# Kernel optimization log

Measured on AMD Instinct MI355X. Metric: run time of the kernel, lower is better.

## Reference

```python
import jax, jax.numpy as jnp
import numpy as np

B = 2
C = 256
NA = 3  # aspect ratios per location
IMG_H, IMG_W = 800, 1216
FEAT_SHAPES = [(200, 304), (100, 152), (50, 76), (25, 38), (13, 19)]
STRIDES = [4, 8, 16, 32, 64]
SIZES = [32, 64, 128, 256, 512]
RATIOS = np.array([0.5, 1.0, 2.0])
PRE_NMS = 1000
POST_NMS = 1000
NMS_TH = 0.7
MIN_SIZE = 1e-3
BBOX_CLIP = float(np.log(1000.0 / 16.0))
NUM_PER_LEVEL = [h * w * NA for h, w in FEAT_SHAPES]


def _make_anchors():
    out = []
    for (h, w), stride, size in zip(FEAT_SHAPES, STRIDES, SIZES):
        hr = np.sqrt(RATIOS)
        wr = 1.0 / hr
        ws, hs = wr * size, hr * size
        base = np.stack([-ws / 2, -hs / 2, ws / 2, hs / 2], 1)  # [NA,4]
        yy, xx = np.meshgrid(np.arange(h) * stride, np.arange(w) * stride, indexing='ij')
        shifts = np.stack([xx.ravel(), yy.ravel(), xx.ravel(), yy.ravel()], 1)  # [h*w,4]
        out.append((shifts[:, None, :] + base[None, :, :]).reshape(-1, 4))
    return jnp.asarray(np.concatenate(out, 0), jnp.float32)  # [A,4]

ANCHORS = _make_anchors()
# level id of each selected (per-level top-k) anchor is static
LEVELS_SEL = jnp.asarray(
    np.concatenate([np.full(min(PRE_NMS, a), i) for i, a in enumerate(NUM_PER_LEVEL)]),
    jnp.float32)


def conv2d(x, w, b, pad):
    y = jax.lax.conv_general_dilated(x, w, (1, 1), [(pad, pad), (pad, pad)],
                                     dimension_numbers=('NCHW', 'OIHW', 'NCHW'))
    return y + b[None, :, None, None]


def decode(reg, anc):
    # BoxCoder.decode with weights (1,1,1,1)
    wa = anc[..., 2] - anc[..., 0]
    ha = anc[..., 3] - anc[..., 1]
    cxa = anc[..., 0] + 0.5 * wa
    cya = anc[..., 1] + 0.5 * ha
    dx, dy = reg[..., 0], reg[..., 1]
    dw = jnp.minimum(reg[..., 2], BBOX_CLIP)
    dh = jnp.minimum(reg[..., 3], BBOX_CLIP)
    cx = dx * wa + cxa
    cy = dy * ha + cya
    w = jnp.exp(dw) * wa
    h = jnp.exp(dh) * ha
    return jnp.stack([cx - 0.5 * w, cy - 0.5 * h, cx + 0.5 * w, cy + 0.5 * h], -1)


def _nms_select(boxes, scores, valid, lvl_offsets):
    # batched_nms via per-level coordinate offset trick; greedy NMS over IoU matrix
    b = boxes + lvl_offsets[:, None]
    s = jnp.where(valid, scores, -jnp.inf)
    order = jnp.argsort(-s)
    bs = b[order]
    keep = valid[order]
    area = (bs[:, 2] - bs[:, 0]) * (bs[:, 3] - bs[:, 1])
    lt = jnp.maximum(bs[:, None, :2], bs[None, :, :2])
    rb = jnp.minimum(bs[:, None, 2:], bs[None, :, 2:])
    wh = jnp.clip(rb - lt, 0.0)
    inter = wh[..., 0] * wh[..., 1]
    iou = inter / (area[:, None] + area[None, :] - inter + 1e-9)
    K = boxes.shape[0]
    ar = jnp.arange(K)

    def body(i, keep):
        sup = keep[i] & (iou[i] > NMS_TH) & (ar > i)
        return keep & ~sup

    keep = jax.lax.fori_loop(0, K, body, keep)
    keep_orig = jnp.zeros(K, bool).at[order].set(keep)
    ms = jnp.where(keep_orig, scores, -jnp.inf)
    top_s, idx = jax.lax.top_k(ms, POST_NMS)
    return idx, jnp.isfinite(top_s)


def reference(feat0, feat1, feat2, feat3, feat4, conv_w, conv_b, cls_w, cls_b, box_w, box_b):
    logit_l, reg_l = [], []
    for f in (feat0, feat1, feat2, feat3, feat4):
        t = jax.nn.relu(conv2d(f, conv_w, conv_b, 1))
        l = conv2d(t, cls_w, cls_b, 0)   # [B,NA,H,W]
        r = conv2d(t, box_w, box_b, 0)   # [B,NA*4,H,W]
        _, _, H, W = l.shape
        logit_l.append(l.transpose(0, 2, 3, 1).reshape(B, -1))                        # HWC order
        reg_l.append(r.reshape(B, NA, 4, H, W).transpose(0, 3, 4, 1, 2).reshape(B, -1, 4))
    logits = jnp.concatenate(logit_l, 1)   # [B,A]
    regs = jnp.concatenate(reg_l, 1)       # [B,A,4]
    proposals = decode(regs, ANCHORS[None])  # [B,A,4]

    # per-level top-k (pre-NMS)
    sel, off = [], 0
    for a in NUM_PER_LEVEL:
        k = min(PRE_NMS, a)
        _, idx = jax.lax.top_k(logits[:, off:off + a], k)
        sel.append(idx + off)
        off += a
    sel = jnp.concatenate(sel, 1)          # [B,Ksel]
    bi = jnp.arange(B)[:, None]
    sc = logits[bi, sel]
    bx = proposals[bi, sel]

    # clip to image, remove small boxes (mask)
    x0 = jnp.clip(bx[..., 0], 0.0, float(IMG_W))
    y0 = jnp.clip(bx[..., 1], 0.0, float(IMG_H))
    x1 = jnp.clip(bx[..., 2], 0.0, float(IMG_W))
    y1 = jnp.clip(bx[..., 3], 0.0, float(IMG_H))
    bx = jnp.stack([x0, y0, x1, y1], -1)
    valid = ((x1 - x0) >= MIN_SIZE) & ((y1 - y0) >= MIN_SIZE)
    offs = LEVELS_SEL * (float(max(IMG_W, IMG_H)) + 1.0)

    idx2, vout = jax.vmap(lambda b_, s_, v_: _nms_select(b_, s_, v_, offs))(
        jax.lax.stop_gradient(bx), jax.lax.stop_gradient(sc), valid)

    boxes_out = jnp.take_along_axis(bx, idx2[..., None], 1)   # [B,POST_NMS,4]
    scores_out = jnp.take_along_axis(sc, idx2, 1)             # [B,POST_NMS]
    boxes_out = jnp.where(vout[..., None], boxes_out, 0.0)
    scores_out = jnp.where(vout, scores_out, -1e9)
    return boxes_out, scores_out


def setup_inputs() -> dict:
    key = jax.random.key(0)
    ks = jax.random.split(key, 9)
    inp = {}
    for i, (h, w) in enumerate(FEAT_SHAPES):
        inp[f'feat{i}'] = jax.random.normal(ks[i], (B, C, h, w), jnp.float32)
    inp['conv_w'] = jax.random.normal(ks[5], (C, C, 3, 3), jnp.float32) * 0.01
    inp['conv_b'] = jnp.zeros((C,), jnp.float32)
    inp['cls_w'] = jax.random.normal(ks[6], (NA, C, 1, 1), jnp.float32) * 0.01
    inp['cls_b'] = jnp.zeros((NA,), jnp.float32)
    inp['box_w'] = jax.random.normal(ks[7], (NA * 4, C, 1, 1), jnp.float32) * 0.01
    inp['box_b'] = jnp.zeros((NA * 4,), jnp.float32)
    return inp
```

## Files before the change

kernel.cpp:

```cpp
#include <hip/hip_runtime.h>
#include <hip/hip_fp16.h>
#include <stdint.h>
#include <math.h>

typedef unsigned int uint;
typedef unsigned short ushort;
typedef unsigned long long ull;
typedef __attribute__((ext_vector_type(8))) _Float16 f16x8;
typedef __attribute__((ext_vector_type(4))) float f32x4;

#define BATCH 2
#define ATOTAL 242991
#define KSEL 4741
#define NW 75
#define POST_NMS 1000
#define WB_ELEMS (2*8*3*3*2*8*64*8)
#define NPAIRS 2850

__device__ __constant__ int dLoff[5]  = {0,182400,228000,239400,242250};
__device__ __constant__ int dCount[5] = {182400,45600,11400,2850,741};
__device__ __constant__ int dSeg[5]   = {0,1000,2000,3000,4000};
__device__ __constant__ int dSegK[5]  = {1000,1000,1000,1000,741};
__device__ __constant__ int dHc[5]     = {200,100,50,25,13};
__device__ __constant__ int dWc[5]     = {304,152,76,38,19};
__device__ __constant__ int dTilesX[5] = {19,10,5,3,2};
__device__ __constant__ int dCumT[6]   = {0,475,605,640,652,656};
__device__ __constant__ int dStrideC[5]= {4,8,16,32,64};
__device__ __constant__ int dSizeC[5]  = {32,64,128,256,512};

__device__ __forceinline__ uint fkey(float f) {
    uint u = __float_as_uint(f);
    return (u & 0x80000000u) ? ~u : (u | 0x80000000u);
}
__device__ __forceinline__ ushort h2u(__half h) {
    union { __half h; ushort u; } x; x.h = h; return x.u;
}

__global__ __launch_bounds__(256) void wt_kernel(const float* __restrict__ conv_w,
                                                 ushort* __restrict__ wB) {
    int t = blockIdx.x * 256 + threadIdx.x;
    if (t >= WB_ELEMS) return;
    int e    = t & 7;
    int lane = (t >> 3) & 63;
    int nt   = (t >> 9) & 7;
    int pl   = (t >> 12) & 1;
    int r    = t >> 13;
    int dx = r % 3; r /= 3;
    int dy = r % 3; r /= 3;
    int icblk = r & 7;
    int ocg = r >> 3;
    int oc = ocg * 128 + nt * 16 + (lane & 15);
    int ic = icblk * 32 + ((lane >> 4) << 3) + e;
    float v = conv_w[(size_t)oc * 2304 + ic * 9 + dy * 3 + dx];
    __half h = __float2half(v);
    float rr = (v - __half2float(h)) * 1024.0f;
    __half m = __float2half(rr);
    wB[t] = (pl == 0) ? h2u(h) : h2u(m);
}

__global__ __launch_bounds__(512) void conv_mfma_all(
    const float* __restrict__ f0, const float* __restrict__ f1,
    const float* __restrict__ f2, const float* __restrict__ f3,
    const float* __restrict__ f4, const ushort* __restrict__ wB,
    const float* __restrict__ conv_b,
    const float* __restrict__ cls_w, const float* __restrict__ cls_b,
    const float* __restrict__ box_w, const float* __restrict__ box_b,
    float* __restrict__ scoresA, float* __restrict__ boxesA)
{
    const int bidx = blockIdx.x;
    const int b    = blockIdx.y;
    const int tid  = threadIdx.x;

    int lvl = 0;
#pragma unroll
    for (int l = 1; l < 5; ++l) if (bidx >= dCumT[l]) lvl = l;
    const int tile   = bidx - dCumT[lvl];
    const int H      = dHc[lvl], W = dWc[lvl];
    const int TILESX = dTilesX[lvl];
    const int ty0    = (tile / TILESX) * 8;
    const int tx0    = (tile % TILESX) * 16;
    const int HW     = H * W;
    const float* feat = (lvl == 0) ? f0 : (lvl == 1) ? f1 : (lvl == 2) ? f2 : (lvl == 3) ? f3 : f4;
    const float* fb = feat + (size_t)b * 256 * HW;

    __shared__ __align__(16) char uni[72192];
    ushort* halo = (ushort*)uni;
    ushort* ldsB = (ushort*)(uni + 23040);
    float*  tS   = (float*)uni;
    float*  hw2  = (float*)(uni + 32768);
    double* houtD= (double*)uni;

    const int lane = tid & 63, wave = tid >> 6;
    const int wm = wave >> 1, wn = wave & 1;
    const int g = lane >> 4, col = lane & 15;
    const int laneA = g * 1440 + col * 8;

    int  hdst[12]; int hoff[12]; bool hval[12];
#pragma unroll
    for (int j = 0; j < 12; ++j) {
        int e = tid + j * 512;
        hdst[j] = -1; hoff[j] = 0; hval[j] = false;
        if (e < 5760) {
            int ic = e / 180, rem = e - ic * 180;
            int hrow = rem / 18, hcol = rem - hrow * 18;
            int gy = ty0 + hrow - 1, gx = tx0 + hcol - 1;
            hdst[j] = (((ic >> 3) * 10 + hrow) * 18 + hcol) * 8 + (ic & 7);
            if (gy >= 0 && gy < H && gx >= 0 && gx < W) {
                hval[j] = true; hoff[j] = ic * HW + gy * W + gx;
            }
        }
    }

    double hacc[4] = {0,0,0,0};

    uint4 Br0, Br1, Br2, Br3, Br4, Br5;
    {
        const uint4* gq = (const uint4*)wB;
        Br0 = gq[tid];        Br1 = gq[tid + 512];
        Br2 = gq[tid + 1024]; Br3 = gq[tid + 1536];
        Br4 = gq[tid + 2048]; Br5 = gq[tid + 2560];
    }

#pragma unroll 1
    for (int ocg = 0; ocg < 2; ++ocg) {
        f32x4 accH[2][4], accM[2][4];
#pragma unroll
        for (int mi = 0; mi < 2; ++mi)
#pragma unroll
            for (int ni = 0; ni < 4; ++ni) {
                accH[mi][ni] = (f32x4){0.f, 0.f, 0.f, 0.f};
                accM[mi][ni] = (f32x4){0.f, 0.f, 0.f, 0.f};
            }

#pragma unroll 1
        for (int s = 0; s < 24; ++s) {
            const int icblk = s / 3;
            const int dy    = s - icblk * 3;

            __syncthreads();
            if (dy == 0) {
                float hv[12];
                const float* fcb = fb + (size_t)icblk * 32 * HW;
#pragma unroll
                for (int j = 0; j < 12; ++j)
                    hv[j] = hval[j] ? fcb[hoff[j]] : 0.f;
#pragma unroll
                for (int j = 0; j < 12; ++j) {
                    if (hdst[j] >= 0) {
                        float v = hv[j];
                        __half h = __float2half(v);
                        float rr = (v - __half2float(h)) * 1024.0f;
                        __half m = __float2half(rr);
                        int li = hdst[j];
                        halo[li] = h2u(h); halo[5760 + li] = h2u(m);
                    }
                }
            }
            {
                uint4* lq = (uint4*)ldsB;
                lq[tid] = Br0;         lq[tid + 512]  = Br1;
                lq[tid + 1024] = Br2;  lq[tid + 1536] = Br3;
                lq[tid + 2048] = Br4;  lq[tid + 2560] = Br5;
            }
            __syncthreads();
            {
                int gstep = ocg * 24 + s + 1;
                if (gstep < 48) {
                    const uint4* gq = (const uint4*)(wB + (size_t)gstep * 24576);
                    Br0 = gq[tid];        Br1 = gq[tid + 512];
                    Br2 = gq[tid + 1024]; Br3 = gq[tid + 1536];
                    Br4 = gq[tid + 2048]; Br5 = gq[tid + 2560];
                }
            }
#pragma unroll 1
            for (int dx = 0; dx < 3; ++dx) {
                f16x8 Ah[2], Am[2];
                const int abase = laneA + dx * 8 + (2 * wm + dy) * 144;
#pragma unroll
                for (int mi = 0; mi < 2; ++mi) {
                    Ah[mi] = *(const f16x8*)(halo + abase + mi * 144);
                    Am[mi] = *(const f16x8*)(halo + 5760 + abase + mi * 144);
                }
#pragma unroll
                for (int ni = 0; ni < 4; ++ni) {
                    const int nt = 4 * wn + ni;
                    f16x8 Bh = *(const f16x8*)(ldsB + (size_t)(dx * 16 + nt) * 512 + lane * 8);
                    f16x8 Bm = *(const f16x8*)(ldsB + (size_t)(dx * 16 + 8 + nt) * 512 + lane * 8);
                    __builtin_amdgcn_s_setprio(1);
#pragma unroll
                    for (int mi = 0; mi < 2; ++mi) {
                        f32x4 cH = accH[mi][ni];
                        f32x4 cM = accM[mi][ni];
                        cH = __builtin_amdgcn_mfma_f32_16x16x32_f16(Ah[mi], Bh, cH, 0, 0, 0);
                        cM = __builtin_amdgcn_mfma_f32_16x16x32_f16(Ah[mi], Bm, cM, 0, 0, 0);
                        cM = __builtin_amdgcn_mfma_f32_16x16x32_f16(Am[mi], Bh, cM, 0, 0, 0);
                        accH[mi][ni] = cH;
                        accM[mi][ni] = cM;
                    }
                    __builtin_amdgcn_s_setprio(0);
                }
            }
        }
        __syncthreads();
        float cb[4];
#pragma unroll
        for (int ni = 0; ni < 4; ++ni)
            cb[ni] = conv_b[ocg * 128 + (4 * wn + ni) * 16 + col];

#pragma unroll 1
        for (int s2 = 0; s2 < 2; ++s2) {
            if (wn == s2) {
#pragma unroll
                for (int mi = 0; mi < 2; ++mi) {
#pragma unroll
                    for (int r = 0; r < 4; ++r) {
                        int px = (2 * wm + mi) * 16 + 4 * g + r;
                        int sw = px & 15;
#pragma unroll
                        for (int ni = 0; ni < 4; ++ni) {
                            int slot = (ni * 4 + (col >> 2)) ^ sw;
                            float val = accH[mi][ni][r] + accM[mi][ni][r] * 0.0009765625f;
                            tS[px * 64 + slot * 4 + (col & 3)] =
                                fmaxf(val + cb[ni], 0.f);
                        }
                    }
                }
            }
            if (tid < 256) {
                const int oc2 = tid >> 2;
                const int h0  = (tid & 3) * 4;
                const int oc  = ocg * 128 + s2 * 64 + oc2;
                float vv[4];
#pragma unroll
                for (int q = 0; q < 4; ++q) {
                    int h = h0 + q;
                    vv[q] = (h < 3) ? cls_w[h * 256 + oc]
                          : (h < 15) ? box_w[(h - 3) * 256 + oc] : 0.f;
                }
                *(float4*)&hw2[oc2 * 16 + h0] = make_float4(vv[0], vv[1], vv[2], vv[3]);
            }
            __syncthreads();
            {
                const int px = tid & 127;
                const int hh = tid >> 7;
                const int sw = px & 15;
#pragma unroll 1
                for (int j4 = 0; j4 < 16; ++j4) {
                    float4 t4 = *(const float4*)&tS[px * 64 + (j4 ^ sw) * 4];
                    float tv[4] = {t4.x, t4.y, t4.z, t4.w};
#pragma unroll
                    for (int jj = 0; jj < 4; ++jj) {
                        const float* hb = &hw2[(j4 * 4 + jj) * 16 + hh * 4];
                        float4 h0 = *(const float4*)hb;
                        double tv_d = (double)tv[jj];
                        hacc[0] += tv_d * (double)h0.x;
                        hacc[1] += tv_d * (double)h0.y;
                        hacc[2] += tv_d * (double)h0.z;
                        hacc[3] += tv_d * (double)h0.w;
                    }
                }
            }
            __syncthreads();
        }
    }

    {
        const int px = tid & 127;
        const int hh = tid >> 7;
#pragma unroll
        for (int j = 0; j < 4; ++j) houtD[px * 16 + hh * 4 + j] = hacc[j];
    }
    __syncthreads();

    if (tid < 128) {
        const int px = tid;
        const int gy = ty0 + (px >> 4);
        const int gx = tx0 + (px & 15);
        if (gy < H && gx < W) {
            const int STRIDE = dStrideC[lvl];
            const int SZ     = dSizeC[lvl];
            const int LOFF   = dLoff[lvl];
#pragma unroll 1
            for (int a = 0; a < 3; ++a) {
                double score = houtD[px * 16 + a] + (double)cls_b[a];
                double rg0 = houtD[px * 16 + 3 + a * 4 + 0] + (double)box_b[a * 4 + 0];
                double rg1 = houtD[px * 16 + 3 + a * 4 + 1] + (double)box_b[a * 4 + 1];
                double rg2 = houtD[px * 16 + 3 + a * 4 + 2] + (double)box_b[a * 4 + 2];
                double rg3 = houtD[px * 16 + 3 + a * 4 + 3] + (double)box_b[a * 4 + 3];
                double ratio = (a == 0) ? 0.5 : ((a == 1) ? 1.0 : 2.0);
                double hr = sqrt(ratio), wr = 1.0 / hr;
                double wsd = wr * (double)SZ, hsd = hr * (double)SZ;
                double sx = (double)(gx * STRIDE), sy = (double)(gy * STRIDE);
                float ax0 = (float)(sx - 0.5 * wsd);
                float ay0 = (float)(sy - 0.5 * hsd);
                float ax1 = (float)(sx + 0.5 * wsd);
                float ay1 = (float)(sy + 0.5 * hsd);
                double wa = (double)ax1 - (double)ax0, ha = (double)ay1 - (double)ay0;
                double cxa = (double)ax0 + 0.5 * wa, cya = (double)ay0 + 0.5 * ha;
                double dwv = fmin(rg2, 4.135166556742356);
                double dhv = fmin(rg3, 4.135166556742356);
                double cx = rg0 * wa + cxa, cy = rg1 * ha + cya;
                double w = exp(dwv) * wa, h = exp(dhv) * ha;
                double x0 = cx - 0.5 * w, y0 = cy - 0.5 * h;
                double x1 = cx + 0.5 * w, y1 = cy + 0.5 * h;
                x0 = fmin(fmax(x0, 0.0), 1216.0);
                y0 = fmin(fmax(y0, 0.0), 800.0);
                x1 = fmin(fmax(x1, 0.0), 1216.0);
                y1 = fmin(fmax(y1, 0.0), 800.0);
                int gidx = LOFF + (gy * W + gx) * 3 + a;
                scoresA[(size_t)b * ATOTAL + gidx] = (float)score;
                float4 bx = make_float4((float)x0, (float)y0, (float)x1, (float)y1);
                *(float4*)&boxesA[((size_t)b * ATOTAL + gidx) * 4] = bx;
            }
        }
    }
}

__global__ __launch_bounds__(1024) void topk_kernel(
    const float* __restrict__ scoresA, const float* __restrict__ boxesA,
    float* __restrict__ selScore, float* __restrict__ selBox,
    int* __restrict__ selValid, int* __restrict__ selAnchor)
{
    const int lvl = blockIdx.x, b = blockIdx.y;
    const int n = dCount[lvl], loff = dLoff[lvl], seg = dSeg[lvl], k = dSegK[lvl];
    const float* sc = scoresA + (size_t)b * ATOTAL + loff;
    const int tid = threadIdx.x;

    float* oS = selScore + b * KSEL;
    float* oB = selBox + (size_t)b * KSEL * 4;
    int* oV = selValid + b * KSEL;
    int* oA = selAnchor + b * KSEL;

    auto emit = [&](int slot, int i) {
        int g = loff + i;
        float s = sc[i];
        float4 bx = *(const float4*)&boxesA[((size_t)b * ATOTAL + g) * 4];
        oS[seg + slot] = s;
        *(float4*)&oB[(size_t)(seg + slot) * 4] = bx;
        oV[seg + slot] = ((bx.z - bx.x) >= 1e-3f && (bx.w - bx.y) >= 1e-3f) ? 1 : 0;
        oA[seg + slot] = g;
    };

    if (n <= k) {
        for (int i = tid; i < n; i += 1024) emit(i, i);
        return;
    }

    __shared__ uint hist[2048];
    __shared__ uint suf[2][1024];
    __shared__ uint sh_bin, sh_krem;
    __shared__ uint cntG, cntE;
    __shared__ int stash[64];

    uint krem = (uint)k;
    uint prefix = 0;
    for (int pass = 0; pass < 3; ++pass) {
        for (int e = tid; e < 2048; e += 1024) hist[e] = 0;
        __syncthreads();
        for (int i = tid; i < n; i += 1024) {
            uint key = fkey(sc[i]);
            uint bin; bool sel;
            if (pass == 0)      { sel = true;                      bin = key >> 21; }
            else if (pass == 1) { sel = ((key >> 21) == prefix);   bin = (key >> 10) & 0x7FFu; }
            else                { sel = ((key >> 10) == prefix);   bin = key & 0x3FFu; }
            if (sel) atomicAdd(&hist[bin], 1u);
        }
        __syncthreads();
        {
            const int nb = (pass == 2) ? 1024 : 2048;
            uint pv = 0;
            if (2 * tid < nb)     pv += hist[2 * tid];
            if (2 * tid + 1 < nb) pv += hist[2 * tid + 1];
            suf[0][tid] = pv;
            __syncthreads();
            int src = 0;
#pragma unroll
            for (int off2 = 1; off2 < 1024; off2 <<= 1) {
                uint v = suf[src][tid] + ((tid + off2 < 1024) ? suf[src][tid + off2] : 0u);
                suf[src ^ 1][tid] = v;
                __syncthreads();
                src ^= 1;
            }
            uint SUFt1 = (tid + 1 < 1024) ? suf[src][tid + 1] : 0u;
            uint h1 = (2 * tid + 1 < nb) ? hist[2 * tid + 1] : 0u;
            if (2 * tid + 1 < nb && SUFt1 < krem && SUFt1 + h1 >= krem) {
                sh_bin = (uint)(2 * tid + 1); sh_krem = krem - SUFt1;
            }
            uint S0 = SUFt1 + h1;
            if (2 * tid < nb) {
                uint h0 = hist[2 * tid];
                if (S0 < krem && S0 + h0 >= krem) {
                    sh_bin = (uint)(2 * tid); sh_krem = krem - S0;
                }
            }
        }
        __syncthreads();
        uint bin = sh_bin; krem = sh_krem;
        if (pass == 0)      prefix = bin;
        else if (pass == 1) prefix = (prefix << 11) | bin;
        else                prefix = (prefix << 10) | bin;
        __syncthreads();
    }
    const uint T = prefix;
    const uint need_eq = krem;
    if (tid == 0) { cntG = 0; cntE = 0; }
    __syncthreads();
    for (int i = tid; i < n; i += 1024) {
        uint key = fkey(sc[i]);
        if (key > T) {
            uint pos = atomicAdd(&cntG, 1u);
            emit((int)pos, i);
        } else if (key == T) {
            uint e = atomicAdd(&cntE, 1u);
            if (e < 64) stash[e] = i;
        }
    }
    __syncthreads();
    if (tid == 0) {
        uint ne = cntE < 64u ? cntE : 64u;
        uint base = cntG;
        for (uint t2 = 0; t2 < need_eq; ++t2) {
            int best = -1, bj = -1;
            for (uint j2 = 0; j2 < ne; ++j2) {
                int v = stash[j2];
                if (v >= 0 && (best < 0 || v < best)) { best = v; bj = j2; }
            }
            if (bj >= 0) { stash[bj] = -1; emit((int)(base + t2), best); }
            else emit((int)(base + t2), 0);
        }
    }
}

__global__ __launch_bounds__(1024) void sort_kernel(
    const float* __restrict__ selScore, const float* __restrict__ selBox,
    const int* __restrict__ selValid, const int* __restrict__ selAnchor,
    int* __restrict__ sortedSlot, float* __restrict__ sortedBoxOff,
    ull* __restrict__ validMask)
{
    const int b = blockIdx.x, tid = threadIdx.x;
    __shared__ ull  skey[8192];
    __shared__ uint spay[8192];
    __shared__ ull  svm[NW];

    for (int i = tid; i < 8192; i += 1024) {
        ull kk2; uint pp;
        if (i < KSEL) {
            float s = selScore[b * KSEL + i];
            int v = selValid[b * KSEL + i];
            uint k32 = v ? fkey(s) : 0x007FFFFFu;
            uint a32 = 0xFFFFFFFFu - (uint)selAnchor[b * KSEL + i];
            kk2 = ((ull)k32 << 32) | a32; pp = (uint)i;
        } else { kk2 = 0ull; pp = 0xFFFFFFFFu; }
        skey[i] = kk2; spay[i] = pp;
    }
    __syncthreads();
    for (uint kk = 2; kk <= 8192; kk <<= 1) {
        for (uint j = kk >> 1; j > 0; j >>= 1) {
            for (int i = tid; i < 8192; i += 1024) {
                uint ixj = (uint)i ^ j;
                if (ixj > (uint)i) {
                    bool up = ((((uint)i) & kk) == 0);
                    ull a = skey[i], c = skey[ixj];
                    bool sw = up ? (a < c) : (a > c);
                    if (sw) {
                        skey[i] = c; skey[ixj] = a;
                        uint tp = spay[i]; spay[i] = spay[ixj]; spay[ixj] = tp;
                    }
                }
            }
            __syncthreads();
        }
    }
    for (int i = tid; i < NW; i += 1024) svm[i] = 0ull;
    __syncthreads();
    for (int i = tid; i < KSEL; i += 1024) {
        uint slot = spay[i];
        sortedSlot[b * KSEL + i] = (int)slot;
        int v = selValid[b * KSEL + slot];
        if (v) atomicOr(&svm[i >> 6], 1ull << (i & 63));
        int lvl = (int)slot / 1000;
        float off = 1217.0f * (float)lvl;
        float4 bx = *(const float4*)&selBox[((size_t)b * KSEL + slot) * 4];
        bx.x += off; bx.y += off; bx.z += off; bx.w += off;
        *(float4*)&sortedBoxOff[((size_t)b * KSEL + i) * 4] = bx;
    }
    __syncthreads();
    for (int i = tid; i < NW; i += 1024) validMask[b * NW + i] = svm[i];
}

__global__ __launch_bounds__(64) void nms_mask(const float* __restrict__ sortedBoxOff,
                                               ull* __restrict__ mat)
{
    const int b = blockIdx.y;
    const int tid = threadIdx.x;
    int rem = blockIdx.x, ib = 0;
    while (rem >= NW - ib) { rem -= NW - ib; ++ib; }
    const int jb = ib + rem;

    __shared__ float4 bj[64];
    __shared__ float  aj[64];
    const int j0 = jb * 64;
    const int jn = (KSEL - j0) < 64 ? (KSEL - j0) : 64;
    if (tid < jn) {
        float4 v = *(const float4*)&sortedBoxOff[((size_t)b * KSEL + j0 + tid) * 4];
        bj[tid] = v; aj[tid] = (v.z - v.x) * (v.w - v.y);
    }
    __syncthreads();
    const int i = ib * 64 + tid;
    if (i >= KSEL) return;
    float4 bi = *(const float4*)&sortedBoxOff[((size_t)b * KSEL + i) * 4];
    float ai = (bi.z - bi.x) * (bi.w - bi.y);
    ull m = 0ull;
    for (int jj = 0; jj < jn; ++jj) {
        int j = j0 + jj;
        if (j <= i) continue;
        float4 bb = bj[jj];
        float ltx = fmaxf(bi.x, bb.x), lty = fmaxf(bi.y, bb.y);
        float rbx = fminf(bi.z, bb.z), rby = fminf(bi.w, bb.w);
        float wx = fmaxf(rbx - ltx, 0.f), wy = fmaxf(rby - lty, 0.f);
        float inter = wx * wy;
        float iou = inter / (ai + aj[jj] - inter + 1e-9f);
        if (iou > 0.7f) m |= (1ull << jj);
    }
    mat[((size_t)b * KSEL + i) * NW + jb] = m;
}

#define LOADG(RA, RB, G) { int base0 = (G) * 16; \
    _Pragma("unroll") for (int d = 0; d < 16; ++d) { int i = base0 + d; \
        RA[d] = (i < KSEL) ? mb[(size_t)i * NW + lane] : 0ull; \
        RB[d] = (hasHi && i < KSEL) ? mb[(size_t)i * NW + 64 + lane] : 0ull; } }
#define PROCG(RA, RB, G) { int base0 = (G) * 16; \
    _Pragma("unroll") for (int d = 0; d < 16; ++d) { int i = base0 + d; \
        if (i < KSEL) { int wi = i >> 6; \
            ull act0 = v0 & ~s0, act1 = v1 & ~s1; \
            ull aw = (wi < 64) ? __shfl(act0, wi, 64) : __shfl(act1, wi - 64, 64); \
            if ((aw >> (i & 63)) & 1ull) { \
                s0 |= (lane >= wi) ? RA[d] : 0ull; \
                s1 |= (lane + 64 >= wi) ? RB[d] : 0ull; \
                if (lane == 0) keptPos[b * POST_NMS + nk] = i; \
                ++nk; \
                if (nk == POST_NMS) { if (lane == 0) nkOut[b] = nk; return; } } } } }

__global__ __launch_bounds__(64) void nms_scan(const ull* __restrict__ mat,
                                               const ull* __restrict__ validMask,
                                               int* __restrict__ keptPos,
                                               int* __restrict__ nkOut)
{
    const int b = blockIdx.x, lane = threadIdx.x;
    const bool hasHi = lane < NW - 64;
    ull v0 = validMask[b * NW + lane];
    ull v1 = hasHi ? validMask[b * NW + 64 + lane] : 0ull;
    ull s0 = 0ull, s1 = 0ull;
    int nk = 0;
    const ull* mb = mat + (size_t)b * KSEL * NW;
    const int NG = (KSEL + 15) / 16;

    ull A0[16], B0[16], A1[16], B1[16];
    LOADG(A0, B0, 0);
    for (int g = 0; g < NG; g += 2) {
        if (g + 1 < NG) LOADG(A1, B1, g + 1);
        PROCG(A0, B0, g);
        if (g + 2 < NG) LOADG(A0, B0, g + 2);
        if (g + 1 < NG) PROCG(A1, B1, g + 1);
    }
    if (lane == 0) nkOut[b] = nk;
}

__global__ __launch_bounds__(256) void out_kernel(
    const int* __restrict__ keptPos, const int* __restrict__ nkOut,
    const int* __restrict__ sortedSlot,
    const float* __restrict__ selBox, const float* __restrict__ selScore,
    float* __restrict__ out)
{
    int t = blockIdx.x * 256 + threadIdx.x;
    if (t >= BATCH * POST_NMS) return;
    int b = t / POST_NMS, row = t - b * POST_NMS;
    float4 bx = make_float4(0.f, 0.f, 0.f, 0.f);
    float sc = -1e9f;
    if (row < nkOut[b]) {
        int i = keptPos[b * POST_NMS + row];
        int slot = sortedSlot[b * KSEL + i];
        bx = *(const float4*)&selBox[((size_t)b * KSEL + slot) * 4];
        sc = selScore[b * KSEL + slot];
    }
    *(float4*)&out[(size_t)t * 4] = bx;
    out[BATCH * POST_NMS * 4 + t] = sc;
}

extern "C" void kernel_launch(void* const* d_in, const int* in_sizes, int n_in,
                              void* d_out, int out_size, void* d_ws, size_t ws_size,
                              hipStream_t stream)
{
    (void)in_sizes; (void)n_in; (void)out_size; (void)ws_size;
    const float* feat[5] = {(const float*)d_in[0], (const float*)d_in[1],
                            (const float*)d_in[2], (const float*)d_in[3],
                            (const float*)d_in[4]};
    const float* conv_w = (const float*)d_in[5];
    const float* conv_b = (const float*)d_in[6];
    const float* cls_w  = (const float*)d_in[7];
    const float* cls_b  = (const float*)d_in[8];
    const float* box_w  = (const float*)d_in[9];
    const float* box_b  = (const float*)d_in[10];
    float* out = (float*)d_out;

    char* ws = (char*)d_ws;
    size_t off = 0;
    auto carve = [&](size_t bytes) -> void* {
        void* p = (void*)(ws + off);
        off += (bytes + 255) & ~(size_t)255;
        return p;
    };
    ushort* wB         = (ushort*)carve((size_t)WB_ELEMS * 2);
    float* scoresA     = (float*)carve((size_t)BATCH * ATOTAL * 4);
    float* boxesA      = (float*)carve((size_t)BATCH * ATOTAL * 16);
    float* selScore    = (float*)carve((size_t)BATCH * KSEL * 4);
    float* selBox      = (float*)carve((size_t)BATCH * KSEL * 16);
    int*   selValid    = (int*)  carve((size_t)BATCH * KSEL * 4);
    int*   selAnchor   = (int*)  carve((size_t)BATCH * KSEL * 4);
    int*   sortedSlot  = (int*)  carve((size_t)BATCH * KSEL * 4);
    float* sortedBoxOff= (float*)carve((size_t)BATCH * KSEL * 16);
    ull*   validMask   = (ull*)  carve((size_t)BATCH * NW * 8);
    ull*   mat         = (ull*)  carve((size_t)BATCH * KSEL * NW * 8);
    int*   keptPos     = (int*)  carve((size_t)BATCH * POST_NMS * 4);
    int*   nkOut       = (int*)  carve(64);

    wt_kernel<<<(WB_ELEMS + 255) / 256, 256, 0, stream>>>(conv_w, wB);

    conv_mfma_all<<<dim3(656, BATCH), 512, 0, stream>>>(
        feat[0], feat[1], feat[2], feat[3], feat[4], wB, conv_b,
        cls_w, cls_b, box_w, box_b, scoresA, boxesA);

    topk_kernel<<<dim3(5, BATCH), 1024, 0, stream>>>(scoresA, boxesA, selScore, selBox, selValid, selAnchor);
    sort_kernel<<<dim3(BATCH), 1024, 0, stream>>>(selScore, selBox, selValid, selAnchor, sortedSlot, sortedBoxOff, validMask);
    nms_mask<<<dim3(NPAIRS, BATCH), 64, 0, stream>>>(sortedBoxOff, mat);
    nms_scan<<<dim3(BATCH), 64, 0, stream>>>(mat, validMask, keptPos, nkOut);
    out_kernel<<<dim3((BATCH * POST_NMS + 255) / 256), 256, 0, stream>>>(keptPos, nkOut, sortedSlot, selBox, selScore, out);
}
```

Before: 1.479 ms.

## Double conv tile height to 16 rows and drop register weight prefetch

Raises the conv tile from 8x16 to 16x16 pixels per block, so each wave computes four M-subtiles instead of two. Every weight fragment loaded into LDS is then reused across twice as many pixels, and the block count roughly halves. The change also removes the register-held prefetch of the next weight step in favour of a direct load-then-store each step, and drops the s_setprio hints. The risks are more accumulator registers and LDS per block, lower occupancy, and exposed global-load latency for the weights.

Result: no change. 1.482 ms (+0.2%).

```diff
diff --git a/kernel.cpp b/kernel.cpp
--- a/kernel.cpp
+++ b/kernel.cpp
@@ -16,6 +16,7 @@
 #define POST_NMS 1000
 #define WB_ELEMS (2*8*3*3*2*8*64*8)
 #define NPAIRS 2850
+#define NTILES 345
 
 __device__ __constant__ int dLoff[5]  = {0,182400,228000,239400,242250};
 __device__ __constant__ int dCount[5] = {182400,45600,11400,2850,741};
@@ -24,7 +25,7 @@
 __device__ __constant__ int dHc[5]     = {200,100,50,25,13};
 __device__ __constant__ int dWc[5]     = {304,152,76,38,19};
 __device__ __constant__ int dTilesX[5] = {19,10,5,3,2};
-__device__ __constant__ int dCumT[6]   = {0,475,605,640,652,656};
+__device__ __constant__ int dCumT[6]   = {0,247,317,337,343,345};
 __device__ __constant__ int dStrideC[5]= {4,8,16,32,64};
 __device__ __constant__ int dSizeC[5]  = {32,64,128,256,512};
 
@@ -77,55 +78,46 @@
     const int tile   = bidx - dCumT[lvl];
     const int H      = dHc[lvl], W = dWc[lvl];
     const int TILESX = dTilesX[lvl];
-    const int ty0    = (tile / TILESX) * 8;
+    const int ty0    = (tile / TILESX) * 16;
     const int tx0    = (tile % TILESX) * 16;
     const int HW     = H * W;
     const float* feat = (lvl == 0) ? f0 : (lvl == 1) ? f1 : (lvl == 2) ? f2 : (lvl == 3) ? f3 : f4;
     const float* fb = feat + (size_t)b * 256 * HW;
 
-    __shared__ __align__(16) char uni[72192];
+    __shared__ __align__(16) char uni[90624];
     ushort* halo = (ushort*)uni;
-    ushort* ldsB = (ushort*)(uni + 23040);
+    ushort* ldsB = (ushort*)(uni + 41472);
     float*  tS   = (float*)uni;
-    float*  hw2  = (float*)(uni + 32768);
+    float*  hw2  = (float*)(uni + 65536);
     double* houtD= (double*)uni;
 
     const int lane = tid & 63, wave = tid >> 6;
     const int wm = wave >> 1, wn = wave & 1;
     const int g = lane >> 4, col = lane & 15;
-    const int laneA = g * 1440 + col * 8;
-
-    int  hdst[12]; int hoff[12]; bool hval[12];
-#pragma unroll
-    for (int j = 0; j < 12; ++j) {
+    const int laneA = g * 2592 + col * 8;
+
+    int hoff[21]; uint hvm = 0;
+#pragma unroll
+    for (int j = 0; j < 21; ++j) {
         int e = tid + j * 512;
-        hdst[j] = -1; hoff[j] = 0; hval[j] = false;
-        if (e < 5760) {
-            int ic = e / 180, rem = e - ic * 180;
+        hoff[j] = 0;
+        if (e < 10368) {
+            int ic = e / 324, rem = e - ic * 324;
             int hrow = rem / 18, hcol = rem - hrow * 18;
             int gy = ty0 + hrow - 1, gx = tx0 + hcol - 1;
-            hdst[j] = (((ic >> 3) * 10 + hrow) * 18 + hcol) * 8 + (ic & 7);
             if (gy >= 0 && gy < H && gx >= 0 && gx < W) {
-                hval[j] = true; hoff[j] = ic * HW + gy * W + gx;
-            }
-        }
-    }
-
-    double hacc[4] = {0,0,0,0};
-
-    uint4 Br0, Br1, Br2, Br3, Br4, Br5;
-    {
-        const uint4* gq = (const uint4*)wB;
-        Br0 = gq[tid];        Br1 = gq[tid + 512];
-        Br2 = gq[tid + 1024]; Br3 = gq[tid + 1536];
-        Br4 = gq[tid + 2048]; Br5 = gq[tid + 2560];
-    }
+                hvm |= (1u << j); hoff[j] = ic * HW + gy * W + gx;
+            }
+        }
+    }
+
+    double hacc[8] = {0,0,0,0,0,0,0,0};
 
 #pragma unroll 1
     for (int ocg = 0; ocg < 2; ++ocg) {
-        f32x4 accH[2][4], accM[2][4];
-#pragma unroll
-        for (int mi = 0; mi < 2; ++mi)
+        f32x4 accH[4][4], accM[4][4];
+#pragma unroll
+        for (int mi = 0; mi < 4; ++mi)
 #pragma unroll
             for (int ni = 0; ni < 4; ++ni) {
                 accH[mi][ni] = (f32x4){0.f, 0.f, 0.f, 0.f};
@@ -139,56 +131,52 @@
 
             __syncthreads();
             if (dy == 0) {
-                float hv[12];
+                float hv[21];
                 const float* fcb = fb + (size_t)icblk * 32 * HW;
 #pragma unroll
-                for (int j = 0; j < 12; ++j)
-                    hv[j] = hval[j] ? fcb[hoff[j]] : 0.f;
-#pragma unroll
-                for (int j = 0; j < 12; ++j) {
-                    if (hdst[j] >= 0) {
+                for (int j = 0; j < 21; ++j)
+                    hv[j] = ((hvm >> j) & 1u) ? fcb[hoff[j]] : 0.f;
+#pragma unroll
+                for (int j = 0; j < 21; ++j) {
+                    int e = tid + j * 512;
+                    if (e < 10368) {
+                        int ic = e / 324, rem = e - ic * 324;
+                        int hrow = rem / 18, hcol = rem - hrow * 18;
+                        int li = (((ic >> 3) * 18 + hrow) * 18 + hcol) * 8 + (ic & 7);
                         float v = hv[j];
                         __half h = __float2half(v);
                         float rr = (v - __half2float(h)) * 1024.0f;
-                        __half m = __float2half(rr);
-                        int li = hdst[j];
-                        halo[li] = h2u(h); halo[5760 + li] = h2u(m);
+                        halo[li] = h2u(h); halo[10368 + li] = h2u(__float2half(rr));
                     }
                 }
             }
             {
+                const uint4* gq = (const uint4*)(wB + (size_t)(ocg * 24 + s) * 24576);
+                uint4 b0 = gq[tid],        b1 = gq[tid + 512],
+                      b2 = gq[tid + 1024], b3 = gq[tid + 1536],
+                      b4 = gq[tid + 2048], b5 = gq[tid + 2560];
                 uint4* lq = (uint4*)ldsB;
-                lq[tid] = Br0;         lq[tid + 512]  = Br1;
-                lq[tid + 1024] = Br2;  lq[tid + 1536] = Br3;
-                lq[tid + 2048] = Br4;  lq[tid + 2560] = Br5;
+                lq[tid] = b0;         lq[tid + 512]  = b1;
+                lq[tid + 1024] = b2;  lq[tid + 1536] = b3;
+                lq[tid + 2048] = b4;  lq[tid + 2560] = b5;
             }
             __syncthreads();
-            {
-                int gstep = ocg * 24 + s + 1;
-                if (gstep < 48) {
-                    const uint4* gq = (const uint4*)(wB + (size_t)gstep * 24576);
-                    Br0 = gq[tid];        Br1 = gq[tid + 512];
-                    Br2 = gq[tid + 1024]; Br3 = gq[tid + 1536];
-                    Br4 = gq[tid + 2048]; Br5 = gq[tid + 2560];
-                }
-            }
 #pragma unroll 1
             for (int dx = 0; dx < 3; ++dx) {
-                f16x8 Ah[2], Am[2];
-                const int abase = laneA + dx * 8 + (2 * wm + dy) * 144;
-#pragma unroll
-                for (int mi = 0; mi < 2; ++mi) {
-                    Ah[mi] = *(const f16x8*)(halo + abase + mi * 144);
-                    Am[mi] = *(const f16x8*)(halo + 5760 + abase + mi * 144);
+                f16x8 Ah[4], Am[4];
+                const int ab = laneA + dx * 8 + (4 * wm + dy) * 144;
+#pragma unroll
+                for (int mi = 0; mi < 4; ++mi) {
+                    Ah[mi] = *(const f16x8*)(halo + ab + mi * 144);
+                    Am[mi] = *(const f16x8*)(halo + 10368 + ab + mi * 144);
                 }
 #pragma unroll
                 for (int ni = 0; ni < 4; ++ni) {
                     const int nt = 4 * wn + ni;
                     f16x8 Bh = *(const f16x8*)(ldsB + (size_t)(dx * 16 + nt) * 512 + lane * 8);
                     f16x8 Bm = *(const f16x8*)(ldsB + (size_t)(dx * 16 + 8 + nt) * 512 + lane * 8);
-                    __builtin_amdgcn_s_setprio(1);
-#pragma unroll
-                    for (int mi = 0; mi < 2; ++mi) {
+#pragma unroll
+                    for (int mi = 0; mi < 4; ++mi) {
                         f32x4 cH = accH[mi][ni];
                         f32x4 cM = accM[mi][ni];
                         cH = __builtin_amdgcn_mfma_f32_16x16x32_f16(Ah[mi], Bh, cH, 0, 0, 0);
@@ -197,7 +185,6 @@
                         accH[mi][ni] = cH;
                         accM[mi][ni] = cM;
                     }
-                    __builtin_amdgcn_s_setprio(0);
                 }
             }
         }
@@ -211,10 +198,10 @@
         for (int s2 = 0; s2 < 2; ++s2) {
             if (wn == s2) {
 #pragma unroll
-                for (int mi = 0; mi < 2; ++mi) {
+                for (int mi = 0; mi < 4; ++mi) {
 #pragma unroll
                     for (int r = 0; r < 4; ++r) {
-                        int px = (2 * wm + mi) * 16 + 4 * g + r;
+                        int px = (4 * wm + mi) * 16 + 4 * g + r;
                         int sw = px & 15;
 #pragma unroll
                         for (int ni = 0; ni < 4; ++ni) {
@@ -241,8 +228,8 @@
             }
             __syncthreads();
             {
-                const int px = tid & 127;
-                const int hh = tid >> 7;
+                const int px = tid & 255;
+                const int hh = tid >> 8;
                 const int sw = px & 15;
 #pragma unroll 1
                 for (int j4 = 0; j4 < 16; ++j4) {
@@ -250,13 +237,18 @@
                     float tv[4] = {t4.x, t4.y, t4.z, t4.w};
 #pragma unroll
                     for (int jj = 0; jj < 4; ++jj) {
-                        const float* hb = &hw2[(j4 * 4 + jj) * 16 + hh * 4];
+                        const float* hb = &hw2[(j4 * 4 + jj) * 16 + hh * 8];
                         float4 h0 = *(const float4*)hb;
+                        float4 h1 = *(const float4*)(hb + 4);
                         double tv_d = (double)tv[jj];
                         hacc[0] += tv_d * (double)h0.x;
                         hacc[1] += tv_d * (double)h0.y;
                         hacc[2] += tv_d * (double)h0.z;
                         hacc[3] += tv_d * (double)h0.w;
+                        hacc[4] += tv_d * (double)h1.x;
+                        hacc[5] += tv_d * (double)h1.y;
+                        hacc[6] += tv_d * (double)h1.z;
+                        hacc[7] += tv_d * (double)h1.w;
                     }
                 }
             }
@@ -265,14 +257,14 @@
     }
 
     {
-        const int px = tid & 127;
-        const int hh = tid >> 7;
-#pragma unroll
-        for (int j = 0; j < 4; ++j) houtD[px * 16 + hh * 4 + j] = hacc[j];
+        const int px = tid & 255;
+        const int hh = tid >> 8;
+#pragma unroll
+        for (int j = 0; j < 8; ++j) houtD[px * 16 + hh * 8 + j] = hacc[j];
     }
     __syncthreads();
 
-    if (tid < 128) {
+    if (tid < 256) {
         const int px = tid;
         const int gy = ty0 + (px >> 4);
         const int gx = tx0 + (px & 15);
@@ -626,7 +618,7 @@
 
     wt_kernel<<<(WB_ELEMS + 255) / 256, 256, 0, stream>>>(conv_w, wB);
 
-    conv_mfma_all<<<dim3(656, BATCH), 512, 0, stream>>>(
+    conv_mfma_all<<<dim3(NTILES, BATCH), 512, 0, stream>>>(
         feat[0], feat[1], feat[2], feat[3], feat[4], wB, conv_b,
         cls_w, cls_b, box_w, box_b, scoresA, boxesA);
 
```

## Double-buffer conv weight tiles in LDS and drop per-step barrier

Applied to the files above, without the earlier changes.

Splits the LDS weight staging area into two buffers so the next step's weight tile is written while the current one is consumed. This cuts the barriers to one per step, except at halo reload points. It also moves the halo staging to the end of every third step and removes the s_setprio hints around the MFMA blocks. The LDS allocation grows from about 72 KB to about 121 KB per block, which likely cuts resident blocks per CU and reduces latency hiding.

After: 1.602 ms. 1.08x slower.

```diff
diff --git a/kernel.cpp b/kernel.cpp
--- a/kernel.cpp
+++ b/kernel.cpp
@@ -83,12 +83,13 @@
     const float* feat = (lvl == 0) ? f0 : (lvl == 1) ? f1 : (lvl == 2) ? f2 : (lvl == 3) ? f3 : f4;
     const float* fb = feat + (size_t)b * 256 * HW;
 
-    __shared__ __align__(16) char uni[72192];
-    ushort* halo = (ushort*)uni;
-    ushort* ldsB = (ushort*)(uni + 23040);
-    float*  tS   = (float*)uni;
-    float*  hw2  = (float*)(uni + 32768);
-    double* houtD= (double*)uni;
+    __shared__ __align__(16) char uni[121344];
+    ushort* halo  = (ushort*)uni;
+    ushort* ldsB0 = (ushort*)(uni + 23040);
+    ushort* ldsB1 = (ushort*)(uni + 72192);
+    float*  tS    = (float*)uni;
+    float*  hw2   = (float*)(uni + 32768);
+    double* houtD = (double*)uni;
 
     const int lane = tid & 63, wave = tid >> 6;
     const int wm = wave >> 1, wn = wave & 1;
@@ -114,12 +115,37 @@
     double hacc[4] = {0,0,0,0};
 
     uint4 Br0, Br1, Br2, Br3, Br4, Br5;
-    {
-        const uint4* gq = (const uint4*)wB;
+
+    auto loadB = [&](int gstep) {
+        const uint4* gq = (const uint4*)(wB + (size_t)gstep * 24576);
         Br0 = gq[tid];        Br1 = gq[tid + 512];
         Br2 = gq[tid + 1024]; Br3 = gq[tid + 1536];
         Br4 = gq[tid + 2048]; Br5 = gq[tid + 2560];
-    }
+    };
+    auto writeB = [&](ushort* dst) {
+        uint4* lq = (uint4*)dst;
+        lq[tid] = Br0;         lq[tid + 512]  = Br1;
+        lq[tid + 1024] = Br2;  lq[tid + 1536] = Br3;
+        lq[tid + 2048] = Br4;  lq[tid + 2560] = Br5;
+    };
+    auto stageHalo = [&](int icb) {
+        float hv[12];
+        const float* fcb = fb + (size_t)icb * 32 * HW;
+#pragma unroll
+        for (int j = 0; j < 12; ++j)
+            hv[j] = hval[j] ? fcb[hoff[j]] : 0.f;
+#pragma unroll
+        for (int j = 0; j < 12; ++j) {
+            if (hdst[j] >= 0) {
+                float v = hv[j];
+                __half h = __float2half(v);
+                float rr = (v - __half2float(h)) * 1024.0f;
+                __half m = __float2half(rr);
+                int li = hdst[j];
+                halo[li] = h2u(h); halo[5760 + li] = h2u(m);
+            }
+        }
+    };
 
 #pragma unroll 1
     for (int ocg = 0; ocg < 2; ++ocg) {
@@ -131,47 +157,21 @@
                 accH[mi][ni] = (f32x4){0.f, 0.f, 0.f, 0.f};
                 accM[mi][ni] = (f32x4){0.f, 0.f, 0.f, 0.f};
             }
+
+        __syncthreads();
+        stageHalo(0);
+        loadB(ocg * 24);
+        writeB(ldsB0);
+        __syncthreads();
+        loadB(ocg * 24 + 1);
+        int cur = 0;
 
 #pragma unroll 1
         for (int s = 0; s < 24; ++s) {
             const int icblk = s / 3;
             const int dy    = s - icblk * 3;
-
-            __syncthreads();
-            if (dy == 0) {
-                float hv[12];
-                const float* fcb = fb + (size_t)icblk * 32 * HW;
-#pragma unroll
-                for (int j = 0; j < 12; ++j)
-                    hv[j] = hval[j] ? fcb[hoff[j]] : 0.f;
-#pragma unroll
-                for (int j = 0; j < 12; ++j) {
-                    if (hdst[j] >= 0) {
-                        float v = hv[j];
-                        __half h = __float2half(v);
-                        float rr = (v - __half2float(h)) * 1024.0f;
-                        __half m = __float2half(rr);
-                        int li = hdst[j];
-                        halo[li] = h2u(h); halo[5760 + li] = h2u(m);
-                    }
-                }
-            }
-            {
-                uint4* lq = (uint4*)ldsB;
-                lq[tid] = Br0;         lq[tid + 512]  = Br1;
-                lq[tid + 1024] = Br2;  lq[tid + 1536] = Br3;
-                lq[tid + 2048] = Br4;  lq[tid + 2560] = Br5;
-            }
-            __syncthreads();
-            {
-                int gstep = ocg * 24 + s + 1;
-                if (gstep < 48) {
-                    const uint4* gq = (const uint4*)(wB + (size_t)gstep * 24576);
-                    Br0 = gq[tid];        Br1 = gq[tid + 512];
-                    Br2 = gq[tid + 1024]; Br3 = gq[tid + 1536];
-                    Br4 = gq[tid + 2048]; Br5 = gq[tid + 2560];
-                }
-            }
+            ushort* Bcur = cur ? ldsB1 : ldsB0;
+
 #pragma unroll 1
             for (int dx = 0; dx < 3; ++dx) {
                 f16x8 Ah[2], Am[2];
@@ -184,9 +184,8 @@
 #pragma unroll
                 for (int ni = 0; ni < 4; ++ni) {
                     const int nt = 4 * wn + ni;
-                    f16x8 Bh = *(const f16x8*)(ldsB + (size_t)(dx * 16 + nt) * 512 + lane * 8);
-                    f16x8 Bm = *(const f16x8*)(ldsB + (size_t)(dx * 16 + 8 + nt) * 512 + lane * 8);
-                    __builtin_amdgcn_s_setprio(1);
+                    f16x8 Bh = *(const f16x8*)(Bcur + (size_t)(dx * 16 + nt) * 512 + lane * 8);
+                    f16x8 Bm = *(const f16x8*)(Bcur + (size_t)(dx * 16 + 8 + nt) * 512 + lane * 8);
 #pragma unroll
                     for (int mi = 0; mi < 2; ++mi) {
                         f32x4 cH = accH[mi][ni];
@@ -197,11 +196,19 @@
                         accH[mi][ni] = cH;
                         accM[mi][ni] = cM;
                     }
-                    __builtin_amdgcn_s_setprio(0);
                 }
             }
-        }
-        __syncthreads();
+            if (s < 23) writeB(cur ? ldsB0 : ldsB1);
+            if (s < 23 && ((s + 1) % 3 == 0)) {
+                __syncthreads();
+                stageHalo(icblk + 1);
+                __syncthreads();
+            } else {
+                __syncthreads();
+            }
+            if (s < 22) loadB(ocg * 24 + s + 2);
+            cur ^= 1;
+        }
         float cb[4];
 #pragma unroll
         for (int ni = 0; ni < 4; ++ni)
```
